# Kernel tuning notes

Measured on AMD Instinct MI355X. Metric: run time of the kernel, lower is better.

The kernel has to match this reference:

```python
import jax, jax.numpy as jnp
import numpy as np

DIM = 512
HEADS = 8
HEAD_DIM = 64
MAX_FREQ = 256.0


def axial_freqs(H, W, head_dim, max_freq=MAX_FREQ):
    # rotary-embedding-torch: per-axis rotary dim = head_dim // 2, freqs_for='pixel'
    r = head_dim // 2
    base = jnp.linspace(1.0, max_freq / 2.0, r // 2) * jnp.pi  # (r/2,)
    ph = jnp.linspace(-1.0, 1.0, H)
    pw = jnp.linspace(-1.0, 1.0, W)
    fh = jnp.repeat(ph[:, None] * base[None, :], 2, axis=-1)  # (H, r) interleaved repeat
    fw = jnp.repeat(pw[:, None] * base[None, :], 2, axis=-1)  # (W, r)
    fh = jnp.broadcast_to(fh[:, None, :], (H, W, r))
    fw = jnp.broadcast_to(fw[None, :, :], (H, W, r))
    return jnp.concatenate([fh, fw], axis=-1)  # (H, W, head_dim)


def rotate_half(t):
    # interleaved pairs: (x1, x2) -> (-x2, x1)
    shp = t.shape
    t = t.reshape(*shp[:-1], -1, 2)
    return jnp.stack((-t[..., 1], t[..., 0]), axis=-1).reshape(shp)


def apply_rope(t, freqs):
    # freqs: (H, W, d) broadcast over (BT, h, H, W, d)
    return t * jnp.cos(freqs) + rotate_half(t) * jnp.sin(freqs)


def setup_inputs() -> dict:
    key = jax.random.key(0)
    k1, k2, k3 = jax.random.split(key, 3)
    B, T, H, W, D = 2, 8, 32, 32, DIM
    inner = HEADS * HEAD_DIM
    x = jax.random.normal(k1, (B, T, H, W, D), dtype=jnp.float32)
    w_qkv = jax.random.normal(k2, (3 * inner, D), dtype=jnp.float32) * (D ** -0.5)
    w_out = jax.random.normal(k3, (D, inner), dtype=jnp.float32) * (inner ** -0.5)
    b_out = jnp.zeros((D,), dtype=jnp.float32)
    return {"x": x, "w_qkv": w_qkv, "w_out": w_out, "b_out": b_out}


def reference(x, w_qkv, w_out, b_out):
    B, T, H, W, D = x.shape
    h, d = HEADS, HEAD_DIM
    qkv = jnp.einsum('bthwc,fc->bthwf', x, w_qkv)  # (B,T,H,W,3*inner)
    q, k, v = jnp.split(qkv, 3, axis=-1)

    def to_heads(t):
        # B T H W (h d) -> (B T) h H W d
        t = t.reshape(B * T, H, W, h, d)
        return jnp.transpose(t, (0, 3, 1, 2, 4))

    q, k, v = to_heads(q), to_heads(k), to_heads(v)
    freqs = axial_freqs(H, W, d)
    q = apply_rope(q, freqs)
    k = apply_rope(k, freqs)

    q = q.reshape(B * T, h, H * W, d)
    k = k.reshape(B * T, h, H * W, d)
    v = v.reshape(B * T, h, H * W, d)

    scale = d ** -0.5
    logits = jnp.einsum('bhnd,bhmd->bhnm', q, k) * scale
    attn = jax.nn.softmax(logits, axis=-1)
    out = jnp.einsum('bhnm,bhmd->bhnd', attn, v)  # (BT, h, HW, d)

    # (B T) h (H W) d -> B T H W (h d)
    out = out.reshape(B, T, h, H, W, d)
    out = jnp.transpose(out, (0, 1, 3, 4, 2, 5)).reshape(B, T, H, W, h * d)
    return jnp.einsum('bthwf,df->bthwd', out, w_out) + b_out
```

## Files before the change

### kernel.cpp

```cpp
#include <hip/hip_runtime.h>
#include <math.h>

#define NH 8
#define HD 64
#define NSEQ 1024
#define DMODEL 512
#define F3 1536
#define NTOK 16384
#define BH 128
#define KVP 72
#define TP 136
#define QSCALE 0.1803368867f

typedef __attribute__((ext_vector_type(8))) short bf16x8;
typedef __attribute__((ext_vector_type(4))) float f32x4;
typedef __attribute__((ext_vector_type(16))) float f32x16;
typedef __attribute__((ext_vector_type(4))) unsigned int u32x4;
#define MFMA16(a, b, c) __builtin_amdgcn_mfma_f32_16x16x32_bf16(a, b, c, 0, 0, 0)
#define MFMA32(a, b, c) __builtin_amdgcn_mfma_f32_32x32x16_bf16(a, b, c, 0, 0, 0)

__device__ __forceinline__ float freq_of(int j) {
    return 3.14159265358979323846f * (1.0f + (float)j * (127.0f / 15.0f));
}
__device__ __forceinline__ unsigned short bf16_rtn(float x) {
    unsigned u = __builtin_bit_cast(unsigned, x);
    return (unsigned short)((u + 0x7FFF + ((u >> 16) & 1)) >> 16);
}
__device__ __forceinline__ int swz(int r) { return (r & 3) ^ ((r >> 2) & 3); }

__global__ __launch_bounds__(256) void cvt2_kernel(
        const float* __restrict__ wq, unsigned short* __restrict__ wq_bf,
        const float* __restrict__ wo, unsigned short* __restrict__ wo_bf) {
    const int b = blockIdx.x;
    const float* src;
    unsigned short* dst;
    int i;
    if (b < F3 * DMODEL / 1024) { src = wq; dst = wq_bf; i = b * 256 + threadIdx.x; }
    else { src = wo; dst = wo_bf; i = (b - F3 * DMODEL / 1024) * 256 + threadIdx.x; }
    const float4 v = ((const float4*)src)[i];
    ((ushort4*)dst)[i] = make_ushort4(bf16_rtn(v.x), bf16_rtn(v.y),
                                      bf16_rtn(v.z), bf16_rtn(v.w));
}

template<int PLANES, int NREP>
__device__ __forceinline__ void gemm_reg_pipe(
        const unsigned short* __restrict__ a_hi, const unsigned short* __restrict__ a_lo,
        const unsigned short* __restrict__ b_bf,
        char* lds, int m0, int f0, int t, f32x4 (&acc)[NREP][4][4]) {
    const int w = t >> 6, lane = t & 63, l15 = lane & 15, quad = lane >> 4;
    const int mw = (w & 1) * 64, nw = (w >> 1) * 64;
    const int APL = PLANES - 1;
    const int NPL = APL + NREP;
    const int STAGE = NPL * 4096;
    const int r = t >> 1;
    const int g0 = (t & 1) * 2;

    uint4 regs[NPL][2];
    auto load_regs = [&](int kt) {
        const int k0 = kt * 32;
        #pragma unroll
        for (int p = 0; p < NPL; p++) {
            const unsigned short* src = (p < APL) ? (p == 0 ? a_hi : a_lo) : b_bf;
            const int row0 = (p < APL) ? m0 : (f0 + (p - APL) * 128);
            const unsigned short* g = src + (size_t)(row0 + r) * DMODEL + k0 + g0 * 8;
            regs[p][0] = *(const uint4*)g;
            regs[p][1] = *(const uint4*)(g + 8);
        }
    };
    auto store_lds = [&](int stage) {
        unsigned short* S = (unsigned short*)lds + stage * STAGE;
        const int s0 = ((g0 ^ swz(r))) * 8;
        const int s1 = (((g0 + 1) ^ swz(r))) * 8;
        #pragma unroll
        for (int p = 0; p < NPL; p++) {
            unsigned short* Sp = S + p * 4096 + r * 32;
            *(uint4*)&Sp[s0] = regs[p][0];
            *(uint4*)&Sp[s1] = regs[p][1];
        }
    };

    load_regs(0);
    store_lds(0);
    for (int kt = 0; kt < 16; kt++) {
        __syncthreads();
        if (kt < 15) load_regs(kt + 1);
        const unsigned short* S = (const unsigned short*)lds + (kt & 1) * STAGE;
        bf16x8 ah[4], al[4];
        #pragma unroll
        for (int mt = 0; mt < 4; mt++) {
            const int rr = mw + mt * 16 + l15;
            const int off = rr * 32 + (quad ^ swz(rr)) * 8;
            ah[mt] = *(const bf16x8*)&S[off];
            if (APL == 2) al[mt] = *(const bf16x8*)&S[4096 + off];
        }
        #pragma unroll
        for (int nr = 0; nr < NREP; nr++) {
            bf16x8 bb[4];
            #pragma unroll
            for (int nt = 0; nt < 4; nt++) {
                const int rr = nw + nt * 16 + l15;
                bb[nt] = *(const bf16x8*)&S[(APL + nr) * 4096 + rr * 32
                                            + (quad ^ swz(rr)) * 8];
            }
            #pragma unroll
            for (int mt = 0; mt < 4; mt++)
                #pragma unroll
                for (int nt = 0; nt < 4; nt++) {
                    acc[nr][mt][nt] = MFMA16(ah[mt], bb[nt], acc[nr][mt][nt]);
                    if (APL == 2) acc[nr][mt][nt] = MFMA16(al[mt], bb[nt], acc[nr][mt][nt]);
                }
        }
        if (kt < 15) store_lds((kt + 1) & 1);
    }
    __syncthreads();
}

__device__ __forceinline__ void gemm_pipe_qkv(
        const float* __restrict__ x, const unsigned short* __restrict__ b_bf,
        char* lds, int m0, int f0, int t, f32x4 (&acc)[2][4][4]) {
    const int w = t >> 6, lane = t & 63, l15 = lane & 15, quad = lane >> 4;
    const int mw = (w & 1) * 64, nw = (w >> 1) * 64;
    const int STAGE = 3 * 4096;
    const int r = t >> 1;
    const int g0 = (t & 1) * 2;

    float4 af[4];
    uint4 bregs[2][2];
    auto load_regs = [&](int kt) {
        const int k0 = kt * 32;
        const float* gA = x + (size_t)(m0 + r) * DMODEL + k0 + g0 * 8;
        #pragma unroll
        for (int i = 0; i < 4; i++) af[i] = ((const float4*)gA)[i];
        #pragma unroll
        for (int p = 0; p < 2; p++) {
            const unsigned short* g =
                b_bf + (size_t)(f0 + p * 128 + r) * DMODEL + k0 + g0 * 8;
            bregs[p][0] = *(const uint4*)g;
            bregs[p][1] = *(const uint4*)(g + 8);
        }
    };
    auto store_lds = [&](int stage) {
        unsigned short* S = (unsigned short*)lds + stage * STAGE;
        const int s0 = ((g0 ^ swz(r))) * 8;
        const int s1 = (((g0 + 1) ^ swz(r))) * 8;
        auto cvt8 = [](const float4 a, const float4 b) {
            const float f[8] = {a.x, a.y, a.z, a.w, b.x, b.y, b.z, b.w};
            unsigned hw[4];
            #pragma unroll
            for (int j = 0; j < 4; j++)
                hw[j] = (unsigned)bf16_rtn(f[2 * j])
                      | ((unsigned)bf16_rtn(f[2 * j + 1]) << 16);
            return make_uint4(hw[0], hw[1], hw[2], hw[3]);
        };
        unsigned short* Sa = S + r * 32;
        *(uint4*)&Sa[s0] = cvt8(af[0], af[1]);
        *(uint4*)&Sa[s1] = cvt8(af[2], af[3]);
        #pragma unroll
        for (int p = 0; p < 2; p++) {
            unsigned short* Sp = S + (1 + p) * 4096 + r * 32;
            *(uint4*)&Sp[s0] = bregs[p][0];
            *(uint4*)&Sp[s1] = bregs[p][1];
        }
    };

    load_regs(0);
    store_lds(0);
    for (int kt = 0; kt < 16; kt++) {
        __syncthreads();
        if (kt < 15) load_regs(kt + 1);
        const unsigned short* S = (const unsigned short*)lds + (kt & 1) * STAGE;
        bf16x8 ah[4];
        #pragma unroll
        for (int mt = 0; mt < 4; mt++) {
            const int rr = mw + mt * 16 + l15;
            ah[mt] = *(const bf16x8*)&S[rr * 32 + (quad ^ swz(rr)) * 8];
        }
        #pragma unroll
        for (int nr = 0; nr < 2; nr++) {
            bf16x8 bb[4];
            #pragma unroll
            for (int nt = 0; nt < 4; nt++) {
                const int rr = nw + nt * 16 + l15;
                bb[nt] = *(const bf16x8*)&S[(1 + nr) * 4096 + rr * 32
                                            + (quad ^ swz(rr)) * 8];
            }
            #pragma unroll
            for (int mt = 0; mt < 4; mt++)
                #pragma unroll
                for (int nt = 0; nt < 4; nt++)
                    acc[nr][mt][nt] = MFMA16(ah[mt], bb[nt], acc[nr][mt][nt]);
        }
        if (kt < 15) store_lds((kt + 1) & 1);
    }
    __syncthreads();
}

__global__ __launch_bounds__(256, 3) void qkv_mfma_kernel(
        const float* __restrict__ x, const unsigned short* __restrict__ wq_bf,
        unsigned short* __restrict__ q_bf, unsigned short* __restrict__ k_bf,
        unsigned short* __restrict__ v_th) {
    __shared__ __align__(16) char lds[49152 + 4608];
    unsigned short* T = (unsigned short*)lds;
    float* t_cy = (float*)(lds + 49152);
    float* t_sy = t_cy + 64;
    float* t_cx = t_sy + 64;
    float* t_sx = t_cx + 512;

    const int m0 = blockIdx.x * 128;
    const int f0 = blockIdx.y * 256;
    const int t = threadIdx.x;
    const int w = t >> 6, lane = t & 63, l15 = lane & 15, quad = lane >> 4;
    const int mw = (w & 1) * 64, nw = (w >> 1) * 64;
    const int sel = f0 >> 9;
    const int bt = m0 >> 10;
    const int n0 = m0 & 1023;

    if (sel != 2) {
        for (int idx = t; idx < 576; idx += 256) {
            if (idx < 64) {
                const int yi = idx >> 4, j = idx & 15;
                const float pos = -1.0f + (float)((n0 >> 5) + yi) * (2.0f / 31.0f);
                float sv, cv; sincosf(pos * freq_of(j), &sv, &cv);
                t_sy[idx] = sv; t_cy[idx] = cv;
            } else {
                const int k2 = idx - 64, xi = k2 >> 4, j = k2 & 15;
                const float pos = -1.0f + (float)xi * (2.0f / 31.0f);
                float sv, cv; sincosf(pos * freq_of(j), &sv, &cv);
                t_sx[k2] = sv; t_cx[k2] = cv;
            }
        }
    }
    __syncthreads();

    f32x4 acc[2][4][4];
    #pragma unroll
    for (int nr = 0; nr < 2; nr++)
        #pragma unroll
        for (int mt = 0; mt < 4; mt++)
            #pragma unroll
            for (int nt = 0; nt < 4; nt++) acc[nr][mt][nt] = (f32x4){0.f, 0.f, 0.f, 0.f};

    gemm_pipe_qkv(x, wq_bf, lds, m0, f0, t, acc);

    #pragma unroll
    for (int nr = 0; nr < 2; nr++) {
        const int fs = f0 + nr * 128;
        if (sel != 2) {
            const float post = (sel == 0) ? QSCALE : 1.0f;
            #pragma unroll
            for (int mt = 0; mt < 4; mt++)
                #pragma unroll
                for (int nt = 0; nt < 4; nt++)
                    #pragma unroll
                    for (int rr = 0; rr < 4; rr++) {
                        const int ml = mw + mt * 16 + quad * 4 + rr;
                        const int dd = (nw + nt * 16 + l15) & 63;
                        const int j0 = (dd & 31) >> 1;
                        float c, s;
                        if (dd < 32) { c = t_cy[(ml >> 5) * 16 + j0]; s = t_sy[(ml >> 5) * 16 + j0]; }
                        else         { c = t_cx[(ml & 31) * 16 + j0]; s = t_sx[(ml & 31) * 16 + j0]; }
                        const float v = acc[nr][mt][nt][rr];
                        const float pv = __shfl_xor(v, 1);
                        acc[nr][mt][nt][rr] =
                            ((l15 & 1) ? (v * c + pv * s) : (v * c - pv * s)) * post;
                    }
        }

        if (sel == 2) {
            #pragma unroll
            for (int mt = 0; mt < 4; mt++)
                #pragma unroll
                for (int nt = 0; nt < 4; nt++) {
                    const int fl = nw + nt * 16 + l15;
                    const int mlb = mw + mt * 16 + quad * 4;
                    ushort4 pk = make_ushort4(
                        bf16_rtn(acc[nr][mt][nt][0]), bf16_rtn(acc[nr][mt][nt][1]),
                        bf16_rtn(acc[nr][mt][nt][2]), bf16_rtn(acc[nr][mt][nt][3]));
                    *(ushort4*)&T[fl * TP + mlb] = pk;
                }
        } else {
            #pragma unroll
            for (int mt = 0; mt < 4; mt++)
                #pragma unroll
                for (int nt = 0; nt < 4; nt++)
                    #pragma unroll
                    for (int rr = 0; rr < 4; rr++) {
                        const int ml = mw + mt * 16 + quad * 4 + rr;
                        const int fl = nw + nt * 16 + l15;
                        T[ml * TP + fl] = bf16_rtn(acc[nr][mt][nt][rr]);
                    }
        }
        __syncthreads();
        if (sel == 2) {
            #pragma unroll
            for (int p = 0; p < 8; p++) {
                const int idx = p * 256 + t;
                const int fl = idx >> 4, g8 = (idx & 15) * 8;
                const int head = ((fs + fl) >> 6) & 7;
                *(uint4*)(v_th + ((size_t)(bt * NH + head) * HD + ((fs + fl) & 63)) * NSEQ
                          + n0 + g8) = *(const uint4*)&T[fl * TP + g8];
            }
        } else {
            unsigned short* dst = (sel == 0) ? q_bf : k_bf;
            #pragma unroll
            for (int p = 0; p < 8; p++) {
                const int idx = p * 256 + t;
                const int ml = idx >> 4, g8 = (idx & 15) * 8;
                const int head = ((fs + g8) >> 6) & 7;
                *(uint4*)(dst + ((size_t)(bt * NH + head) * NSEQ + n0 + ml) * HD
                          + ((fs + g8) & 63)) = *(const uint4*)&T[ml * TP + g8];
            }
        }
        __syncthreads();
    }
}

__global__ __launch_bounds__(512, 2) void attn_kernel(
        const unsigned short* __restrict__ q_bf, const unsigned short* __restrict__ k_bf,
        const unsigned short* __restrict__ v_th,
        unsigned short* __restrict__ o_bf) {
    __shared__ unsigned short Ks[2][64 * KVP];
    __shared__ unsigned short Vs[2][64 * KVP];
    __shared__ float Lsh[256];

    const int bh = blockIdx.x;
    const int qt = blockIdx.y;
    const int t = threadIdx.x;
    const int w = t >> 6;
    const int lane = t & 63;
    const int l31 = lane & 31;
    const int hi = lane >> 5;

    const size_t bh_nd = (size_t)bh * NSEQ * HD;
    const size_t bh_dn = (size_t)bh * HD * NSEQ;

    bf16x8 qfB[4];
    {
        const size_t rbase =
            bh_nd + (size_t)(qt * 256 + w * 32 + l31) * HD + hi * 8;
        #pragma unroll
        for (int ds = 0; ds < 4; ds++)
            qfB[ds] = *(const bf16x8*)(q_bf + rbase + ds * 16);
    }

    const int sr = t >> 3, soff = (t & 7) * 8;
    uint4 kr, vr;
    auto load_kv = [&](int kt) {
        kr = *(const uint4*)(k_bf + bh_nd + (size_t)(kt * 64 + sr) * HD + soff);
        vr = *(const uint4*)(v_th + bh_dn + (size_t)sr * NSEQ + kt * 64 + soff);
    };
    auto store_kv = [&](int st) {
        *(uint4*)&Ks[st][sr * KVP + soff] = kr;
        *(uint4*)&Vs[st][sr * KVP + soff] = vr;
    };

    f32x16 o_acc[2], zero16;
    float l_sum = 0.f;
    #pragma unroll
    for (int i = 0; i < 16; i++) {
        o_acc[0][i] = 0.f; o_acc[1][i] = 0.f; zero16[i] = 0.f;
    }

    load_kv(0);
    store_kv(0);
    for (int kt = 0; kt < 16; kt++) {
        __syncthreads();
        if (kt < 15) load_kv(kt + 1);
        const unsigned short* K = Ks[kt & 1];
        const unsigned short* V = Vs[kt & 1];

        #pragma unroll
        for (int nt2 = 0; nt2 < 2; nt2++) {
            bf16x8 kb[4];
            #pragma unroll
            for (int ds = 0; ds < 4; ds++)
                kb[ds] = *(const bf16x8*)&K[(nt2 * 32 + l31) * KVP + ds * 16 + hi * 8];

            __builtin_amdgcn_s_setprio(1);
            f32x16 s = MFMA32(kb[0], qfB[0], zero16);
            #pragma unroll
            for (int ds = 1; ds < 4; ds++) s = MFMA32(kb[ds], qfB[ds], s);
            __builtin_amdgcn_s_setprio(0);

            unsigned wv[8];
            float pp[8];
            #pragma unroll
            for (int i = 0; i < 8; i++) {
                const float p0 = exp2f(s[2 * i]);
                const float p1 = exp2f(s[2 * i + 1]);
                pp[i] = p0 + p1;
                asm("v_cvt_pk_bf16_f32 %0, %1, %2" : "=v"(wv[i]) : "v"(p0), "v"(p1));
            }
            l_sum += ((pp[0] + pp[1]) + (pp[2] + pp[3]))
                   + ((pp[4] + pp[5]) + (pp[6] + pp[7]));

            asm volatile("v_permlane32_swap_b32 %0, %1" : "+v"(wv[0]), "+v"(wv[2]));
            asm volatile("v_permlane32_swap_b32 %0, %1" : "+v"(wv[1]), "+v"(wv[3]));
            asm volatile("v_permlane32_swap_b32 %0, %1" : "+v"(wv[4]), "+v"(wv[6]));
            asm volatile("v_permlane32_swap_b32 %0, %1" : "+v"(wv[5]), "+v"(wv[7]));

            __builtin_amdgcn_s_setprio(1);
            #pragma unroll
            for (int k2 = 0; k2 < 2; k2++) {
                const u32x4 paw = {wv[k2 * 4 + 0], wv[k2 * 4 + 1],
                                   wv[k2 * 4 + 2], wv[k2 * 4 + 3]};
                const bf16x8 pa = __builtin_bit_cast(bf16x8, paw);
                #pragma unroll
                for (int dt = 0; dt < 2; dt++) {
                    const bf16x8 vb = *(const bf16x8*)&V[(dt * 32 + l31) * KVP
                                         + (nt2 * 2 + k2) * 16 + hi * 8];
                    o_acc[dt] = MFMA32(pa, vb, o_acc[dt]);
                }
            }
            __builtin_amdgcn_s_setprio(0);
        }
        if (kt < 15) store_kv((kt + 1) & 1);
    }

    l_sum += __shfl_xor(l_sum, 32);
    const float inv = 1.0f / l_sum;
    if (hi == 0) Lsh[w * 32 + l31] = inv;
    __syncthreads();

    unsigned short* Osh = &Ks[0][0];
    #pragma unroll
    for (int r = 0; r < 16; r++) {
        const int row32 = (r & 3) + 8 * (r >> 2) + 4 * hi;
        const float invr = Lsh[w * 32 + row32];
        const int row = w * 32 + row32;
        #pragma unroll
        for (int dt = 0; dt < 2; dt++)
            Osh[row * KVP + dt * 32 + l31] = bf16_rtn(o_acc[dt][r] * invr);
    }
    __syncthreads();
    const int btq = bh >> 3, head = bh & 7;
    #pragma unroll
    for (int p = 0; p < 4; p++) {
        const int idx = p * 512 + t;
        const int row = idx >> 3, g8 = (idx & 7) * 8;
        *(uint4*)(o_bf + ((size_t)(btq * NSEQ + qt * 256 + row)) * DMODEL
                  + head * HD + g8) = *(const uint4*)&Osh[row * KVP + g8];
    }
}

__global__ __launch_bounds__(256, 2) void proj_mfma_kernel(
        const unsigned short* __restrict__ o_bf,
        const unsigned short* __restrict__ wo_bf,
        const float* __restrict__ b_out, float* __restrict__ out) {
    __shared__ __align__(16) char lds[49152];

    const int m0 = blockIdx.x * 128;
    const int f0 = blockIdx.y * 256;
    const int t = threadIdx.x;
    const int w = t >> 6, lane = t & 63, l15 = lane & 15, quad = lane >> 4;
    const int mw = (w & 1) * 64, nw = (w >> 1) * 64;

    f32x4 acc[2][4][4];
    #pragma unroll
    for (int nr = 0; nr < 2; nr++)
        #pragma unroll
        for (int mt = 0; mt < 4; mt++)
            #pragma unroll
            for (int nt = 0; nt < 4; nt++) acc[nr][mt][nt] = (f32x4){0.f, 0.f, 0.f, 0.f};

    gemm_reg_pipe<2, 2>(o_bf, o_bf, wo_bf, lds, m0, f0, t, acc);

    #pragma unroll
    for (int nr = 0; nr < 2; nr++) {
        const int fs = f0 + nr * 128;
        float bias_v[4];
        #pragma unroll
        for (int nt = 0; nt < 4; nt++) bias_v[nt] = b_out[fs + nw + nt * 16 + l15];
        #pragma unroll
        for (int mt = 0; mt < 4; mt++)
            #pragma unroll
            for (int nt = 0; nt < 4; nt++)
                #pragma unroll
                for (int rr = 0; rr < 4; rr++) {
                    const int m = m0 + mw + mt * 16 + quad * 4 + rr;
                    out[(size_t)m * DMODEL + fs + nw + nt * 16 + l15] =
                        acc[nr][mt][nt][rr] + bias_v[nt];
                }
    }
}

extern "C" void kernel_launch(void* const* d_in, const int* in_sizes, int n_in,
                              void* d_out, int out_size, void* d_ws, size_t ws_size,
                              hipStream_t stream) {
    const float* x  = (const float*)d_in[0];
    const float* wq = (const float*)d_in[1];
    const float* wo = (const float*)d_in[2];
    const float* bo = (const float*)d_in[3];
    float* out = (float*)d_out;

    const size_t per = (size_t)BH * NSEQ * HD;
    unsigned short* o_bf = (unsigned short*)d_ws;
    unsigned short* q_bf = o_bf + per;
    unsigned short* k_bf = q_bf + per;
    unsigned short* v_th = k_bf + per;
    unsigned short* wq_bf = v_th + per;
    unsigned short* wo_bf = wq_bf + (size_t)F3 * DMODEL;

    cvt2_kernel<<<dim3((F3 * DMODEL + DMODEL * DMODEL) / 1024), 256, 0, stream>>>(
        wq, wq_bf, wo, wo_bf);
    qkv_mfma_kernel<<<dim3(NTOK / 128, F3 / 256), 256, 0, stream>>>(
        x, wq_bf, q_bf, k_bf, v_th);
    attn_kernel<<<dim3(BH, 4), 512, 0, stream>>>(
        q_bf, k_bf, v_th, o_bf);
    proj_mfma_kernel<<<dim3(NTOK / 128, DMODEL / 256), 256, 0, stream>>>(
        o_bf, wo_bf, bo, out);
}
```

Before: 206.8 us.

## Deepen GEMM global-load prefetch to two tiles ahead with double register buffers

Both GEMM pipelines (generic reg-pipe and QKV) now keep two register buffer sets and issue global loads two k-tiles ahead, unrolling the k-loop by two with alternating LDS stages. The goal is to hide global memory latency behind more MFMA work per load. The cost is extra registers for the second buffer set, which may reduce occupancy under the launch bound of 3 blocks per SM or cause spills.

Result: slower. 395.8 us (+91.4%).

```diff
diff --git a/kernel.cpp b/kernel.cpp
--- a/kernel.cpp
+++ b/kernel.cpp
@@ -55,36 +55,31 @@
     const int r = t >> 1;
     const int g0 = (t & 1) * 2;
 
-    uint4 regs[NPL][2];
-    auto load_regs = [&](int kt) {
+    uint4 rA[NPL][2], rB[NPL][2];
+    auto load_regs = [&](uint4 (&rg)[NPL][2], int kt) {
         const int k0 = kt * 32;
         #pragma unroll
         for (int p = 0; p < NPL; p++) {
             const unsigned short* src = (p < APL) ? (p == 0 ? a_hi : a_lo) : b_bf;
             const int row0 = (p < APL) ? m0 : (f0 + (p - APL) * 128);
             const unsigned short* g = src + (size_t)(row0 + r) * DMODEL + k0 + g0 * 8;
-            regs[p][0] = *(const uint4*)g;
-            regs[p][1] = *(const uint4*)(g + 8);
-        }
-    };
-    auto store_lds = [&](int stage) {
+            rg[p][0] = *(const uint4*)g;
+            rg[p][1] = *(const uint4*)(g + 8);
+        }
+    };
+    auto store_lds = [&](uint4 (&rg)[NPL][2], int stage) {
         unsigned short* S = (unsigned short*)lds + stage * STAGE;
         const int s0 = ((g0 ^ swz(r))) * 8;
         const int s1 = (((g0 + 1) ^ swz(r))) * 8;
         #pragma unroll
         for (int p = 0; p < NPL; p++) {
             unsigned short* Sp = S + p * 4096 + r * 32;
-            *(uint4*)&Sp[s0] = regs[p][0];
-            *(uint4*)&Sp[s1] = regs[p][1];
-        }
-    };
-
-    load_regs(0);
-    store_lds(0);
-    for (int kt = 0; kt < 16; kt++) {
-        __syncthreads();
-        if (kt < 15) load_regs(kt + 1);
-        const unsigned short* S = (const unsigned short*)lds + (kt & 1) * STAGE;
+            *(uint4*)&Sp[s0] = rg[p][0];
+            *(uint4*)&Sp[s1] = rg[p][1];
+        }
+    };
+    auto compute = [&](int stage) {
+        const unsigned short* S = (const unsigned short*)lds + stage * STAGE;
         bf16x8 ah[4], al[4];
         #pragma unroll
         for (int mt = 0; mt < 4; mt++) {
@@ -110,7 +105,21 @@
                     if (APL == 2) acc[nr][mt][nt] = MFMA16(al[mt], bb[nt], acc[nr][mt][nt]);
                 }
         }
-        if (kt < 15) store_lds((kt + 1) & 1);
+    };
+
+    load_regs(rA, 0);
+    store_lds(rA, 0);
+    load_regs(rA, 1);
+    for (int kt2 = 0; kt2 < 8; kt2++) {
+        const int kt = kt2 * 2;
+        __syncthreads();
+        if (kt < 14) load_regs(rB, kt + 2);
+        compute(0);
+        store_lds(rA, 1);
+        __syncthreads();
+        if (kt < 13) load_regs(rA, kt + 3);
+        compute(1);
+        if (kt < 14) store_lds(rB, 0);
     }
     __syncthreads();
 }
@@ -124,9 +133,9 @@
     const int r = t >> 1;
     const int g0 = (t & 1) * 2;
 
-    float4 af[4];
-    uint4 bregs[2][2];
-    auto load_regs = [&](int kt) {
+    float4 afA[4], afB[4];
+    uint4 brA[2][2], brB[2][2];
+    auto load_regs = [&](float4 (&af)[4], uint4 (&br)[2][2], int kt) {
         const int k0 = kt * 32;
         const float* gA = x + (size_t)(m0 + r) * DMODEL + k0 + g0 * 8;
         #pragma unroll
@@ -135,11 +144,11 @@
         for (int p = 0; p < 2; p++) {
             const unsigned short* g =
                 b_bf + (size_t)(f0 + p * 128 + r) * DMODEL + k0 + g0 * 8;
-            bregs[p][0] = *(const uint4*)g;
-            bregs[p][1] = *(const uint4*)(g + 8);
-        }
-    };
-    auto store_lds = [&](int stage) {
+            br[p][0] = *(const uint4*)g;
+            br[p][1] = *(const uint4*)(g + 8);
+        }
+    };
+    auto store_lds = [&](float4 (&af)[4], uint4 (&br)[2][2], int stage) {
         unsigned short* S = (unsigned short*)lds + stage * STAGE;
         const int s0 = ((g0 ^ swz(r))) * 8;
         const int s1 = (((g0 + 1) ^ swz(r))) * 8;
@@ -158,17 +167,12 @@
         #pragma unroll
         for (int p = 0; p < 2; p++) {
             unsigned short* Sp = S + (1 + p) * 4096 + r * 32;
-            *(uint4*)&Sp[s0] = bregs[p][0];
-            *(uint4*)&Sp[s1] = bregs[p][1];
-        }
-    };
-
-    load_regs(0);
-    store_lds(0);
-    for (int kt = 0; kt < 16; kt++) {
-        __syncthreads();
-        if (kt < 15) load_regs(kt + 1);
-        const unsigned short* S = (const unsigned short*)lds + (kt & 1) * STAGE;
+            *(uint4*)&Sp[s0] = br[p][0];
+            *(uint4*)&Sp[s1] = br[p][1];
+        }
+    };
+    auto compute = [&](int stage) {
+        const unsigned short* S = (const unsigned short*)lds + stage * STAGE;
         bf16x8 ah[4];
         #pragma unroll
         for (int mt = 0; mt < 4; mt++) {
@@ -190,7 +194,21 @@
                 for (int nt = 0; nt < 4; nt++)
                     acc[nr][mt][nt] = MFMA16(ah[mt], bb[nt], acc[nr][mt][nt]);
         }
-        if (kt < 15) store_lds((kt + 1) & 1);
+    };
+
+    load_regs(afA, brA, 0);
+    store_lds(afA, brA, 0);
+    load_regs(afA, brA, 1);
+    for (int kt2 = 0; kt2 < 8; kt2++) {
+        const int kt = kt2 * 2;
+        __syncthreads();
+        if (kt < 14) load_regs(afB, brB, kt + 2);
+        compute(0);
+        store_lds(afA, brA, 1);
+        __syncthreads();
+        if (kt < 13) load_regs(afA, brA, kt + 3);
+        compute(1);
+        if (kt < 14) store_lds(afB, brB, 0);
     }
     __syncthreads();
 }
```

## Prefetch fp32 activations two k-steps ahead in QKV GEMM pipeline

Applied to the files above, without the earlier changes.

Restructures the QKV projection GEMM main loop so the fp32 x tile is loaded into alternating register sets two k-steps ahead, while the bf16 weight tile stays one step ahead. The loop is unrolled by two with fixed LDS stages, which hides more global-load latency behind the MFMA work. The extra prefetch registers push register pressure up, so launch bounds drop from 3 to 2 blocks per CU, which lowers occupancy.

Result: slower. 260.2 us (+25.8%).

```diff
diff --git a/kernel.cpp b/kernel.cpp
--- a/kernel.cpp
+++ b/kernel.cpp
@@ -124,51 +124,64 @@
     const int r = t >> 1;
     const int g0 = (t & 1) * 2;
 
-    float4 af[4];
-    uint4 bregs[2][2];
-    auto load_regs = [&](int kt) {
-        const int k0 = kt * 32;
-        const float* gA = x + (size_t)(m0 + r) * DMODEL + k0 + g0 * 8;
-        #pragma unroll
-        for (int i = 0; i < 4; i++) af[i] = ((const float4*)gA)[i];
-        #pragma unroll
-        for (int p = 0; p < 2; p++) {
-            const unsigned short* g =
-                b_bf + (size_t)(f0 + p * 128 + r) * DMODEL + k0 + g0 * 8;
-            bregs[p][0] = *(const uint4*)g;
-            bregs[p][1] = *(const uint4*)(g + 8);
-        }
-    };
-    auto store_lds = [&](int stage) {
-        unsigned short* S = (unsigned short*)lds + stage * STAGE;
-        const int s0 = ((g0 ^ swz(r))) * 8;
-        const int s1 = (((g0 + 1) ^ swz(r))) * 8;
-        auto cvt8 = [](const float4 a, const float4 b) {
-            const float f[8] = {a.x, a.y, a.z, a.w, b.x, b.y, b.z, b.w};
-            unsigned hw[4];
-            #pragma unroll
-            for (int j = 0; j < 4; j++)
-                hw[j] = (unsigned)bf16_rtn(f[2 * j])
-                      | ((unsigned)bf16_rtn(f[2 * j + 1]) << 16);
-            return make_uint4(hw[0], hw[1], hw[2], hw[3]);
-        };
-        unsigned short* Sa = S + r * 32;
-        *(uint4*)&Sa[s0] = cvt8(af[0], af[1]);
-        *(uint4*)&Sa[s1] = cvt8(af[2], af[3]);
+    const float* gA = x + (size_t)(m0 + r) * DMODEL + g0 * 8;
+    const unsigned short* gB0 = b_bf + (size_t)(f0 + r) * DMODEL + g0 * 8;
+    const unsigned short* gB1 = b_bf + (size_t)(f0 + 128 + r) * DMODEL + g0 * 8;
+
+    float4 afA[4], afB[4];
+    uint4 br[2][2];
+
+    auto loadA_A = [&](int kt) {
+        const float* g = gA + kt * 32;
+        #pragma unroll
+        for (int i = 0; i < 4; i++) afA[i] = ((const float4*)g)[i];
+    };
+    auto loadA_B = [&](int kt) {
+        const float* g = gA + kt * 32;
+        #pragma unroll
+        for (int i = 0; i < 4; i++) afB[i] = ((const float4*)g)[i];
+    };
+    auto loadBr = [&](int kt) {
+        br[0][0] = *(const uint4*)(gB0 + kt * 32);
+        br[0][1] = *(const uint4*)(gB0 + kt * 32 + 8);
+        br[1][0] = *(const uint4*)(gB1 + kt * 32);
+        br[1][1] = *(const uint4*)(gB1 + kt * 32 + 8);
+    };
+    const int s0 = ((g0 ^ swz(r))) * 8;
+    const int s1 = (((g0 + 1) ^ swz(r))) * 8;
+    auto cvt8 = [](const float4 a, const float4 b) {
+        const float f[8] = {a.x, a.y, a.z, a.w, b.x, b.y, b.z, b.w};
+        unsigned hw[4];
+        #pragma unroll
+        for (int j = 0; j < 4; j++)
+            hw[j] = (unsigned)bf16_rtn(f[2 * j])
+                  | ((unsigned)bf16_rtn(f[2 * j + 1]) << 16);
+        return make_uint4(hw[0], hw[1], hw[2], hw[3]);
+    };
+    auto storeBr = [&](unsigned short* S) {
         #pragma unroll
         for (int p = 0; p < 2; p++) {
             unsigned short* Sp = S + (1 + p) * 4096 + r * 32;
-            *(uint4*)&Sp[s0] = bregs[p][0];
-            *(uint4*)&Sp[s1] = bregs[p][1];
-        }
-    };
-
-    load_regs(0);
-    store_lds(0);
-    for (int kt = 0; kt < 16; kt++) {
-        __syncthreads();
-        if (kt < 15) load_regs(kt + 1);
-        const unsigned short* S = (const unsigned short*)lds + (kt & 1) * STAGE;
+            *(uint4*)&Sp[s0] = br[p][0];
+            *(uint4*)&Sp[s1] = br[p][1];
+        }
+    };
+    auto storeA = [&](int stage) {
+        unsigned short* S = (unsigned short*)lds + stage * STAGE;
+        unsigned short* Sa = S + r * 32;
+        *(uint4*)&Sa[s0] = cvt8(afA[0], afA[1]);
+        *(uint4*)&Sa[s1] = cvt8(afA[2], afA[3]);
+        storeBr(S);
+    };
+    auto storeB = [&](int stage) {
+        unsigned short* S = (unsigned short*)lds + stage * STAGE;
+        unsigned short* Sa = S + r * 32;
+        *(uint4*)&Sa[s0] = cvt8(afB[0], afB[1]);
+        *(uint4*)&Sa[s1] = cvt8(afB[2], afB[3]);
+        storeBr(S);
+    };
+    auto compute = [&](int stage) {
+        const unsigned short* S = (const unsigned short*)lds + stage * STAGE;
         bf16x8 ah[4];
         #pragma unroll
         for (int mt = 0; mt < 4; mt++) {
@@ -190,12 +203,27 @@
                 for (int nt = 0; nt < 4; nt++)
                     acc[nr][mt][nt] = MFMA16(ah[mt], bb[nt], acc[nr][mt][nt]);
         }
-        if (kt < 15) store_lds((kt + 1) & 1);
+    };
+
+    loadA_A(0); loadBr(0); storeA(0);
+    loadA_B(1);
+    for (int kt2 = 0; kt2 < 8; kt2++) {
+        const int kt = kt2 * 2;
+        __syncthreads();
+        if (kt < 15) loadBr(kt + 1);
+        if (kt < 14) loadA_A(kt + 2);
+        compute(0);
+        if (kt < 15) storeB(1);
+        __syncthreads();
+        if (kt < 14) loadBr(kt + 2);
+        if (kt < 13) loadA_B(kt + 3);
+        compute(1);
+        if (kt < 14) storeA(0);
     }
     __syncthreads();
 }
 
-__global__ __launch_bounds__(256, 3) void qkv_mfma_kernel(
+__global__ __launch_bounds__(256, 2) void qkv_mfma_kernel(
         const float* __restrict__ x, const unsigned short* __restrict__ wq_bf,
         unsigned short* __restrict__ q_bf, unsigned short* __restrict__ k_bf,
         unsigned short* __restrict__ v_th) {
```
